# Kernel tuning notes

Hardware: AMD Instinct MI355X
Metric: run time of the kernel (lower is better)

Reference implementation:

```python
import jax, jax.numpy as jnp
import numpy as np

N_USERS = 200000   # == num movies (code indexes movie_x with user ids)
N_MOVIES = 200000
N_ENT = 400000
C = 64


def _ngcf(x, edge_index, W1, b1, W2, b2, num_nodes):
    # PyG flow source_to_target: x_j = x[src], x_i = x[dst], aggr='add' at dst
    src, dst = edge_index[0], edge_index[1]
    xj = x[src]                      # [E, C]
    xi = x[dst]                      # [E, C]
    msg = xj @ W1 + b1 + (xi * xj) @ W2 + b2
    return jax.ops.segment_sum(msg, dst, num_segments=num_nodes)


def _rgcn(x, edge_index, Wrel, Wroot, brgcn, num_nodes):
    # single relation (edge_type all zero); RGCNConv default aggr='mean'
    src, dst = edge_index[0], edge_index[1]
    msg = x[src] @ Wrel              # [E, C]
    agg = jax.ops.segment_sum(msg, dst, num_segments=num_nodes)
    cnt = jax.ops.segment_sum(jnp.ones((msg.shape[0],), msg.dtype), dst,
                              num_segments=num_nodes)
    agg = agg / jnp.maximum(cnt, 1.0)[:, None]
    return agg + x @ Wroot + brgcn


def setup_inputs() -> dict:
    key = jax.random.key(0)
    ks = jax.random.split(key, 12)
    s = 1.0 / np.sqrt(C)
    return {
        "user_x": jax.random.normal(ks[0], (N_USERS, C), jnp.float32),
        "movie_x": jax.random.normal(ks[1], (N_MOVIES, C), jnp.float32),
        "entity_x": jax.random.normal(ks[2], (N_ENT, C), jnp.float32),
        "um_edge_index": jax.random.randint(ks[3], (2, 1000000), 0, N_USERS, jnp.int32),
        "me_edge_index": jax.random.randint(ks[4], (2, 1000000), 0, N_MOVIES, jnp.int32),
        "W1": jax.random.uniform(ks[5], (C, C), jnp.float32, -s, s),
        "b1": jax.random.uniform(ks[6], (C,), jnp.float32, -s, s),
        "W2": jax.random.uniform(ks[7], (C, C), jnp.float32, -s, s),
        "b2": jax.random.uniform(ks[8], (C,), jnp.float32, -s, s),
        "Wrel": jax.random.uniform(ks[9], (C, C), jnp.float32, -s, s),
        "Wroot": jax.random.uniform(ks[10], (C, C), jnp.float32, -s, s),
        "brgcn": jax.random.uniform(ks[11], (C,), jnp.float32, -s, s),
    }


def reference(user_x, movie_x, entity_x, um_edge_index, me_edge_index,
              W1, b1, W2, b2, Wrel, Wroot, brgcn):
    # movie side: NGCF over user->movie edges, x = movie_x (faithful to source)
    movie_msg = _ngcf(movie_x, um_edge_index, W1, b1, W2, b2, N_MOVIES)
    entity_msg = _rgcn(entity_x, me_edge_index, Wrel, Wroot, brgcn, N_ENT)
    movie_emb = jnp.concatenate(
        [movie_x, movie_msg + entity_msg[:N_MOVIES]], axis=1)
    # user side: reversed edges
    um_rev = jnp.stack([um_edge_index[1], um_edge_index[0]], axis=0)
    user_msg = _ngcf(user_x, um_rev, W1, b1, W2, b2, N_USERS)
    user_emb = jnp.concatenate([user_x, user_msg], axis=1)
    return (user_emb, movie_emb)
```

## Files before the change

kernel.cpp:

```cpp
#include <hip/hip_runtime.h>

#define NUSERS  200000
#define NMOVIES 200000
#define NROWS   200000
#define NCB     782
#define NB      512
#define CAPB    1792
#define ELCAP   1792
#define OVF_MAX 8192

typedef __attribute__((ext_vector_type(8))) short bf16x8;
typedef __attribute__((ext_vector_type(4))) float f32x4;

__global__ __launch_bounds__(256) void bin_scatter_kernel(
    const int* __restrict__ um, const int* __restrict__ me,
    int* __restrict__ C, int* __restrict__ LB, int* __restrict__ part,
    int E_um, int E_me, int CH_um, int CH_me)
{
    __shared__ int hist[NCB];
    __shared__ int lscan[NCB];
    __shared__ int tsum[256];
    __shared__ int stage[1984];

    const int bid = blockIdx.x;
    const int s = bid / NB;
    const int blk = bid % NB;
    const int E  = (s < 2) ? E_um : E_me;
    const int CH = (s < 2) ? CH_um : CH_me;
    const int t0 = blk * CH;
    const int n = max(0, min(t0 + CH, E) - t0);
    const int tid = threadIdx.x;

    const int* kp;
    const int* vp;
    if (s == 0)      { kp = um;        vp = um + E_um; }
    else if (s == 1) { kp = um + E_um; vp = um; }
    else             { kp = me + E_me; vp = me; }

    for (int i = tid; i < NCB; i += 256) hist[i] = 0;
    __syncthreads();

    for (int j = tid; j < n; j += 256) {
        const int key = kp[t0 + j];
        atomicAdd(&hist[key >> 8], 1);
    }
    __syncthreads();

    const int crow = (s * NB + blk) * NCB;
    for (int i = tid; i < NCB; i += 256) C[crow + i] = hist[i];

    {
        const int b4 = tid * 4;
        const int v0 = (b4 + 0 < NCB) ? hist[b4 + 0] : 0;
        const int v1 = (b4 + 1 < NCB) ? hist[b4 + 1] : 0;
        const int v2 = (b4 + 2 < NCB) ? hist[b4 + 2] : 0;
        const int v3 = (b4 + 3 < NCB) ? hist[b4 + 3] : 0;
        const int ssum = v0 + v1 + v2 + v3;
        tsum[tid] = ssum;
        __syncthreads();
#pragma unroll
        for (int off = 1; off < 256; off <<= 1) {
            const int t = (tid >= off) ? tsum[tid - off] : 0;
            __syncthreads();
            tsum[tid] += t;
            __syncthreads();
        }
        const int excl = tsum[tid] - ssum;
        if (b4 + 0 < NCB) lscan[b4 + 0] = excl;
        if (b4 + 1 < NCB) lscan[b4 + 1] = excl + v0;
        if (b4 + 2 < NCB) lscan[b4 + 2] = excl + v0 + v1;
        if (b4 + 3 < NCB) lscan[b4 + 3] = excl + v0 + v1 + v2;
    }
    __syncthreads();

    for (int i = tid; i < NCB; i += 256) LB[crow + i] = lscan[i];
    for (int i = tid; i < NCB; i += 256) hist[i] = lscan[i];
    __syncthreads();

    for (int j = tid; j < n; j += 256) {
        const int key = kp[t0 + j];
        const int val = vp[t0 + j];
        const int pos = atomicAdd(&hist[key >> 8], 1);
        stage[pos] = (val << 8) | (key & 255);
    }
    __syncthreads();

    int* preg;
    if (s == 0)      preg = part + (size_t)blk * CH_um;
    else if (s == 1) preg = part + (size_t)NB * CH_um + (size_t)blk * CH_um;
    else             preg = part + (size_t)2 * NB * CH_um + (size_t)blk * CH_me;
    for (int i = tid; i < n; i += 256) preg[i] = stage[i];
}

__global__ __launch_bounds__(256) void bin_csr_kernel(
    const int* __restrict__ part,
    const int* __restrict__ C, const int* __restrict__ LB,
    int* __restrict__ csr,
    int* __restrict__ rowcnt_all,
    int* __restrict__ rowstart_all,
    int* __restrict__ ovf_meta, int* __restrict__ ovf_list,
    int CH_um, int CH_me)
{
    __shared__ int cfrag[NB];
    __shared__ int foff[NB + 1];
    __shared__ int tsum[256];
    __shared__ int el[ELCAP];
    __shared__ int sorted[ELCAP];
    __shared__ int fhist[256];
    __shared__ int frank[256];

    const int bid = blockIdx.x;
    const int s = bid / NCB;
    const int bin = bid % NCB;
    const int tid = threadIdx.x;
    const int CH = (s < 2) ? CH_um : CH_me;
    const int* preg = part + (s == 0 ? (size_t)0
                      : (s == 1 ? (size_t)NB * CH_um
                                : (size_t)2 * NB * CH_um));

    for (int b = tid; b < NB; b += 256) cfrag[b] = C[(s * NB + b) * NCB + bin];
    fhist[tid] = 0;
    __syncthreads();

    {
        const int a0 = cfrag[2 * tid];
        const int a1 = cfrag[2 * tid + 1];
        const int ss = a0 + a1;
        tsum[tid] = ss;
        __syncthreads();
#pragma unroll
        for (int off = 1; off < 256; off <<= 1) {
            const int t = (tid >= off) ? tsum[tid - off] : 0;
            __syncthreads();
            tsum[tid] += t;
            __syncthreads();
        }
        const int excl = tsum[tid] - ss;
        foff[2 * tid] = excl;
        foff[2 * tid + 1] = excl + a0;
        if (tid == 255) foff[NB] = tsum[255];
    }
    __syncthreads();
    const int nbin = foff[NB];
    const int nel = min(nbin, ELCAP);

    for (int b = tid; b < NB; b += 256) {
        const int c = cfrag[b];
        if (c == 0) continue;
        const int off = LB[(s * NB + b) * NCB + bin];
        const int* frag = preg + (size_t)b * CH + off;
        const int dst0 = foff[b];
        for (int j = 0; j < c; ++j) {
            const int v = frag[j];
            const int idx = dst0 + j;
            if (idx < ELCAP) {
                el[idx] = v;
            } else {
                const int i = atomicAdd(ovf_meta, 1);
                if (i < OVF_MAX) {
                    ovf_list[2 * i]     = (s << 18) | (bin * 256 + (v & 255));
                    ovf_list[2 * i + 1] = v >> 8;
                }
            }
        }
    }
    __syncthreads();

    for (int i = tid; i < nel; i += 256) atomicAdd(&fhist[el[i] & 255], 1);
    __syncthreads();

    {
        const int v = fhist[tid];
        tsum[tid] = v;
        __syncthreads();
#pragma unroll
        for (int off = 1; off < 256; off <<= 1) {
            const int t = (tid >= off) ? tsum[tid - off] : 0;
            __syncthreads();
            tsum[tid] += t;
            __syncthreads();
        }
        const int excl = tsum[tid] - v;
        frank[tid] = excl;
        const int r = bin * 256 + tid;
        if (r < NROWS) {
            rowstart_all[s * NROWS + r] = ((s * NCB) + bin) * CAPB + excl;
            rowcnt_all[s * NROWS + r] = v;
        }
    }
    __syncthreads();

    for (int i = tid; i < nel; i += 256) {
        const int p = el[i];
        const int pos = atomicAdd(&frank[p & 255], 1);
        sorted[pos] = p >> 8;
    }
    __syncthreads();

    int* outp = csr + ((size_t)s * NCB + bin) * CAPB;
    for (int i = tid; i < nel; i += 256) outp[i] = sorted[i];
}

__global__ __launch_bounds__(256) void gather_kernel(
    const int* __restrict__ csr,
    const float* __restrict__ x,
    const int* __restrict__ rowcnt,
    const int* __restrict__ rowstart,
    float* __restrict__ outbase,
    int out_off, int nrows)
{
    const int lane = threadIdx.x & 63;
    const int wid = __builtin_amdgcn_readfirstlane(
        (blockIdx.x * blockDim.x + threadIdx.x) >> 6);
    const int nw = (gridDim.x * blockDim.x) >> 6;
    const int rpw = (nrows + nw - 1) / nw;
    const int r0 = wid * rpw;
    const int r1 = min(r0 + rpw, nrows);
    for (int r = r0; r < r1; ++r) {
        const int c = rowcnt[r];
        const int base = rowstart[r];
        float acc0 = 0.f, acc1 = 0.f, acc2 = 0.f, acc3 = 0.f;
        int j = 0;
        for (; j + 4 <= c; j += 4) {
            const int s0 = csr[base + j];
            const int s1 = csr[base + j + 1];
            const int s2 = csr[base + j + 2];
            const int s3 = csr[base + j + 3];
            acc0 += x[(size_t)s0 * 64 + lane];
            acc1 += x[(size_t)s1 * 64 + lane];
            acc2 += x[(size_t)s2 * 64 + lane];
            acc3 += x[(size_t)s3 * 64 + lane];
        }
        for (; j < c; ++j) {
            const int s0 = csr[base + j];
            acc0 += x[(size_t)s0 * 64 + lane];
        }
        outbase[(size_t)r * 128 + out_off + lane] = (acc0 + acc1) + (acc2 + acc3);
    }
}

__global__ __launch_bounds__(256) void fixup_kernel(
    const int* __restrict__ ovf_meta,
    const int* __restrict__ ovf_list,
    const float* __restrict__ user_x,
    const float* __restrict__ movie_x,
    const float* __restrict__ entity_x,
    int* __restrict__ rowcnt_all,
    float* __restrict__ out_user,
    float* __restrict__ out_movie)
{
    const int n = min(ovf_meta[0], OVF_MAX);
    const int lane = threadIdx.x & 63;
    const int wv = (blockIdx.x * blockDim.x + threadIdx.x) >> 6;
    const int nw = (gridDim.x * blockDim.x) >> 6;
    for (int i = wv; i < n; i += nw) {
        const int key = ovf_list[2 * i];
        const int src = ovf_list[2 * i + 1];
        const int s = key >> 18;
        const int dst = key & 0x3FFFF;
        if (dst >= NROWS) continue;
        if (s == 0) {
            atomicAdd(&out_user[(size_t)dst * 128 + 64 + lane],
                      user_x[(size_t)src * 64 + lane]);
        } else if (s == 1) {
            atomicAdd(&out_movie[(size_t)dst * 128 + 64 + lane],
                      movie_x[(size_t)src * 64 + lane]);
        } else {
            atomicAdd(&out_movie[(size_t)dst * 128 + lane],
                      entity_x[(size_t)src * 64 + lane]);
        }
        if (lane == 0) atomicAdd(&rowcnt_all[s * NROWS + dst], 1);
    }
}

__global__ __launch_bounds__(256) void bsplit_kernel(
    const float* __restrict__ W1, const float* __restrict__ W2,
    const float* __restrict__ Wrel, const float* __restrict__ Wroot,
    unsigned short* __restrict__ BH, unsigned short* __restrict__ BL)
{
    const int idx = blockIdx.x * blockDim.x + threadIdx.x;
    if (idx >= 8 * 4 * 64 * 8) return;
    const int j = idx & 7;
    const int f = idx >> 3;
    const int l = f & 63;
    const int t = (f >> 6) & 3;
    const int s = f >> 8;
    const int k = 32 * s + 8 * (l >> 4) + j;
    const int col = 16 * t + (l & 15);
    const float* Wsrc;
    switch (k >> 6) {
        case 0:  Wsrc = W1;    break;
        case 1:  Wsrc = W2;    break;
        case 2:  Wsrc = Wrel;  break;
        default: Wsrc = Wroot; break;
    }
    const float v = Wsrc[(k & 63) * 64 + col];
    const unsigned int bits = __float_as_uint(v);
    const unsigned short h = (unsigned short)(bits >> 16);
    const float rem = v - __uint_as_float((unsigned)h << 16);
    BH[idx] = h;
    BL[idx] = (unsigned short)(__float_as_uint(rem) >> 16);
}

__device__ __forceinline__ short bf_hi(float v, float& rem) {
    const unsigned int b = __float_as_uint(v);
    const unsigned short h = (unsigned short)(b >> 16);
    rem = v - __uint_as_float((unsigned)h << 16);
    return (short)h;
}
__device__ __forceinline__ short bf_tr(float v) {
    return (short)(__float_as_uint(v) >> 16);
}
__device__ __forceinline__ void split8(float4 q0, float4 q1,
                                       bf16x8& Ah, bf16x8& Al) {
    float r0, r1, r2, r3, r4, r5, r6, r7;
    Ah[0] = bf_hi(q0.x, r0); Ah[1] = bf_hi(q0.y, r1);
    Ah[2] = bf_hi(q0.z, r2); Ah[3] = bf_hi(q0.w, r3);
    Ah[4] = bf_hi(q1.x, r4); Ah[5] = bf_hi(q1.y, r5);
    Ah[6] = bf_hi(q1.z, r6); Ah[7] = bf_hi(q1.w, r7);
    Al[0] = bf_tr(r0); Al[1] = bf_tr(r1); Al[2] = bf_tr(r2); Al[3] = bf_tr(r3);
    Al[4] = bf_tr(r4); Al[5] = bf_tr(r5); Al[6] = bf_tr(r6); Al[7] = bf_tr(r7);
}

#define MFMA3(acc, Ah, Al, Bh, Bl)                                           \
    acc = __builtin_amdgcn_mfma_f32_16x16x32_bf16(Ah, Bh, acc, 0, 0, 0);     \
    acc = __builtin_amdgcn_mfma_f32_16x16x32_bf16(Al, Bh, acc, 0, 0, 0);     \
    acc = __builtin_amdgcn_mfma_f32_16x16x32_bf16(Ah, Bl, acc, 0, 0, 0);

__global__ __launch_bounds__(256) void finalize_user_mfma(
    const float* __restrict__ user_x,
    const int* __restrict__ cnt_u,
    const float* __restrict__ b1, const float* __restrict__ b2,
    const unsigned short* __restrict__ BH,
    const unsigned short* __restrict__ BL,
    float* out_user)
{
    const int lane = threadIdx.x & 63;
    const int wv = threadIdx.x >> 6;
    const int sub = lane & 15, grp = lane >> 4;
    const int rbase = blockIdx.x * 64 + wv * 16;
    const int myrow = rbase + sub;

    f32x4 acc0 = {0.f, 0.f, 0.f, 0.f}, acc1 = acc0, acc2 = acc0, acc3 = acc0;

#pragma unroll
    for (int s = 0; s < 4; ++s) {
        float4 q0, q1;
        if (s < 2) {
            const float* p = out_user + (size_t)myrow * 128 + 64 + 32 * s + 8 * grp;
            q0 = *(const float4*)p;
            q1 = *(const float4*)(p + 4);
        } else {
            const int off = 32 * (s - 2) + 8 * grp;
            const float* ps = out_user + (size_t)myrow * 128 + 64 + off;
            const float* px = user_x + (size_t)myrow * 64 + off;
            const float4 s0 = *(const float4*)ps, s1 = *(const float4*)(ps + 4);
            const float4 x0 = *(const float4*)px, x1 = *(const float4*)(px + 4);
            q0.x = s0.x * x0.x; q0.y = s0.y * x0.y;
            q0.z = s0.z * x0.z; q0.w = s0.w * x0.w;
            q1.x = s1.x * x1.x; q1.y = s1.y * x1.y;
            q1.z = s1.z * x1.z; q1.w = s1.w * x1.w;
        }
        bf16x8 Ah, Al;
        split8(q0, q1, Ah, Al);
#pragma unroll
        for (int t = 0; t < 4; ++t) {
            const int fo = ((s * 4 + t) * 64 + lane) * 8;
            const bf16x8 Bh = *(const bf16x8*)(BH + fo);
            const bf16x8 Bl = *(const bf16x8*)(BL + fo);
            if (t == 0) { MFMA3(acc0, Ah, Al, Bh, Bl) }
            else if (t == 1) { MFMA3(acc1, Ah, Al, Bh, Bl) }
            else if (t == 2) { MFMA3(acc2, Ah, Al, Bh, Bl) }
            else { MFMA3(acc3, Ah, Al, Bh, Bl) }
        }
    }

#pragma unroll
    for (int i = 0; i < 4; ++i) {
        const int row = rbase + 4 * i + grp;
        const float4 xv = *(const float4*)(user_x + (size_t)row * 64 + sub * 4);
        *(float4*)(out_user + (size_t)row * 128 + sub * 4) = xv;
    }

#pragma unroll
    for (int t = 0; t < 4; ++t) {
        const int col = 16 * t + sub;
        const float bb = b1[col] + b2[col];
        const f32x4 a = (t == 0) ? acc0 : (t == 1) ? acc1 : (t == 2) ? acc2 : acc3;
#pragma unroll
        for (int r = 0; r < 4; ++r) {
            const int row = rbase + 4 * grp + r;
            out_user[(size_t)row * 128 + 64 + col] =
                a[r] + (float)cnt_u[row] * bb;
        }
    }
}

__global__ __launch_bounds__(256) void finalize_movie_mfma(
    const float* __restrict__ movie_x,
    const float* __restrict__ entity_x,
    const int* __restrict__ cnt_m, const int* __restrict__ cnt_e,
    const float* __restrict__ b1, const float* __restrict__ b2,
    const float* __restrict__ brgcn,
    const unsigned short* __restrict__ BH,
    const unsigned short* __restrict__ BL,
    float* out_movie)
{
    const int lane = threadIdx.x & 63;
    const int wv = threadIdx.x >> 6;
    const int sub = lane & 15, grp = lane >> 4;
    const int rbase = blockIdx.x * 64 + wv * 16;
    const int myrow = rbase + sub;
    const float invce = 1.0f / fmaxf((float)cnt_e[myrow], 1.0f);

    f32x4 acc0 = {0.f, 0.f, 0.f, 0.f}, acc1 = acc0, acc2 = acc0, acc3 = acc0;

#pragma unroll
    for (int s = 0; s < 8; ++s) {
        float4 q0, q1;
        if (s < 2) {
            const float* p = out_movie + (size_t)myrow * 128 + 64 + 32 * s + 8 * grp;
            q0 = *(const float4*)p;
            q1 = *(const float4*)(p + 4);
        } else if (s < 4) {
            const int off = 32 * (s - 2) + 8 * grp;
            const float* ps = out_movie + (size_t)myrow * 128 + 64 + off;
            const float* px = movie_x + (size_t)myrow * 64 + off;
            const float4 s0 = *(const float4*)ps, s1 = *(const float4*)(ps + 4);
            const float4 x0 = *(const float4*)px, x1 = *(const float4*)(px + 4);
            q0.x = s0.x * x0.x; q0.y = s0.y * x0.y;
            q0.z = s0.z * x0.z; q0.w = s0.w * x0.w;
            q1.x = s1.x * x1.x; q1.y = s1.y * x1.y;
            q1.z = s1.z * x1.z; q1.w = s1.w * x1.w;
        } else if (s < 6) {
            const float* p = out_movie + (size_t)myrow * 128 + 32 * (s - 4) + 8 * grp;
            const float4 e0 = *(const float4*)p, e1 = *(const float4*)(p + 4);
            q0.x = e0.x * invce; q0.y = e0.y * invce;
            q0.z = e0.z * invce; q0.w = e0.w * invce;
            q1.x = e1.x * invce; q1.y = e1.y * invce;
            q1.z = e1.z * invce; q1.w = e1.w * invce;
        } else {
            const float* p = entity_x + (size_t)myrow * 64 + 32 * (s - 6) + 8 * grp;
            q0 = *(const float4*)p;
            q1 = *(const float4*)(p + 4);
        }
        bf16x8 Ah, Al;
        split8(q0, q1, Ah, Al);
#pragma unroll
        for (int t = 0; t < 4; ++t) {
            const int fo = ((s * 4 + t) * 64 + lane) * 8;
            const bf16x8 Bh = *(const bf16x8*)(BH + fo);
            const bf16x8 Bl = *(const bf16x8*)(BL + fo);
            if (t == 0) { MFMA3(acc0, Ah, Al, Bh, Bl) }
            else if (t == 1) { MFMA3(acc1, Ah, Al, Bh, Bl) }
            else if (t == 2) { MFMA3(acc2, Ah, Al, Bh, Bl) }
            else { MFMA3(acc3, Ah, Al, Bh, Bl) }
        }
    }

#pragma unroll
    for (int i = 0; i < 4; ++i) {
        const int row = rbase + 4 * i + grp;
        const float4 xv = *(const float4*)(movie_x + (size_t)row * 64 + sub * 4);
        *(float4*)(out_movie + (size_t)row * 128 + sub * 4) = xv;
    }

#pragma unroll
    for (int t = 0; t < 4; ++t) {
        const int col = 16 * t + sub;
        const float bb = b1[col] + b2[col];
        const float br = brgcn[col];
        const f32x4 a = (t == 0) ? acc0 : (t == 1) ? acc1 : (t == 2) ? acc2 : acc3;
#pragma unroll
        for (int r = 0; r < 4; ++r) {
            const int row = rbase + 4 * grp + r;
            out_movie[(size_t)row * 128 + 64 + col] =
                a[r] + (float)cnt_m[row] * bb + br;
        }
    }
}

extern "C" void kernel_launch(void* const* d_in, const int* in_sizes, int n_in,
                              void* d_out, int out_size, void* d_ws, size_t ws_size,
                              hipStream_t stream)
{
    const float* user_x   = (const float*)d_in[0];
    const float* movie_x  = (const float*)d_in[1];
    const float* entity_x = (const float*)d_in[2];
    const int*   um       = (const int*)d_in[3];
    const int*   me       = (const int*)d_in[4];
    const float* W1       = (const float*)d_in[5];
    const float* b1       = (const float*)d_in[6];
    const float* W2       = (const float*)d_in[7];
    const float* b2       = (const float*)d_in[8];
    const float* Wrel     = (const float*)d_in[9];
    const float* Wroot    = (const float*)d_in[10];
    const float* brgcn    = (const float*)d_in[11];

    const int E_um = in_sizes[3] / 2;
    const int E_me = in_sizes[4] / 2;
    const int CH_um = (E_um + NB - 1) / NB;
    const int CH_me = (E_me + NB - 1) / NB;

    float* out_user  = (float*)d_out;
    float* out_movie = out_user + (size_t)NUSERS * 128;

    int* C        = (int*)d_ws;
    int* LB       = C + 3 * NB * NCB;
    int* rowcnt   = LB + 3 * NB * NCB;
    int* rowstart = rowcnt + 3 * NROWS;
    int* ovf_meta = rowstart + 3 * NROWS;
    int* ovf_list = ovf_meta + 2;
    int* part     = ovf_list + 2 * OVF_MAX;
    int* csr      = part + (size_t)2 * NB * CH_um + (size_t)NB * CH_me;
    uintptr_t bp = (uintptr_t)(csr + (size_t)3 * NCB * CAPB);
    bp = (bp + 63) & ~(uintptr_t)63;
    unsigned short* BH = (unsigned short*)bp;
    unsigned short* BL = BH + 16384;

    int* cnt_u = rowcnt;
    int* cnt_m = rowcnt + NROWS;
    int* cnt_e = rowcnt + 2 * NROWS;

    hipMemsetAsync(ovf_meta, 0, 2 * sizeof(int), stream);

    bsplit_kernel<<<64, 256, 0, stream>>>(W1, W2, Wrel, Wroot, BH, BL);
    bin_scatter_kernel<<<3 * NB, 256, 0, stream>>>(um, me, C, LB, part,
                                                   E_um, E_me, CH_um, CH_me);
    bin_csr_kernel<<<3 * NCB, 256, 0, stream>>>(part, C, LB, csr,
                                                rowcnt, rowstart,
                                                ovf_meta, ovf_list,
                                                CH_um, CH_me);

    gather_kernel<<<2048, 256, 0, stream>>>(csr, entity_x,
                                            cnt_e, rowstart + 2 * NROWS,
                                            out_movie, 0, NMOVIES);
    gather_kernel<<<2048, 256, 0, stream>>>(csr, movie_x,
                                            cnt_m, rowstart + NROWS,
                                            out_movie, 64, NMOVIES);
    gather_kernel<<<2048, 256, 0, stream>>>(csr, user_x,
                                            cnt_u, rowstart,
                                            out_user, 64, NUSERS);

    fixup_kernel<<<16, 256, 0, stream>>>(ovf_meta, ovf_list, user_x, movie_x,
                                         entity_x, rowcnt, out_user, out_movie);

    finalize_user_mfma<<<NUSERS / 64, 256, 0, stream>>>(
        user_x, cnt_u, b1, b2, BH, BL, out_user);
    finalize_movie_mfma<<<NMOVIES / 64, 256, 0, stream>>>(
        movie_x, entity_x, cnt_m, cnt_e, b1, b2, brgcn, BH, BL, out_movie);
}
```

Before: 352.7 us.

## Fuse neighbor gather into MFMA finalize kernels via shared-memory tiles

Before, three gather kernels wrote aggregated sums into the output buffer and two finalize kernels read them back for the bf16-split MFMA projection. Now each 16-row wave gathers its neighbor sums straight into a padded shared-memory tile, and the MFMA projection runs in the same kernel. This removes the global write and re-read of the intermediate aggregates. Because of that, overflow edges can no longer be pre-summed, so the fixup kernel now applies the full per-edge W1/W2/Wrel projection before its atomic adds. The CSR builder also counts row histograms over every element, not only the stored ones. The movie NGCF kernel adds onto the RGCN partial already in the output, which makes the kernels order-dependent.

```diff
diff --git a/kernel.cpp b/kernel.cpp
--- a/kernel.cpp
+++ b/kernel.cpp
@@ -97,6 +97,7 @@
     const int* __restrict__ C, const int* __restrict__ LB,
     int* __restrict__ csr,
     int* __restrict__ rowcnt_all,
+    int* __restrict__ rowstored_all,
     int* __restrict__ rowstart_all,
     int* __restrict__ ovf_meta, int* __restrict__ ovf_list,
     int CH_um, int CH_me)
@@ -107,6 +108,7 @@
     __shared__ int el[ELCAP];
     __shared__ int sorted[ELCAP];
     __shared__ int fhist[256];
+    __shared__ int fexcl[256];
     __shared__ int frank[256];
 
     const int bid = blockIdx.x;
@@ -142,7 +144,6 @@
     }
     __syncthreads();
     const int nbin = foff[NB];
-    const int nel = min(nbin, ELCAP);
 
     for (int b = tid; b < NB; b += 256) {
         const int c = cfrag[b];
@@ -152,6 +153,7 @@
         const int dst0 = foff[b];
         for (int j = 0; j < c; ++j) {
             const int v = frag[j];
+            atomicAdd(&fhist[v & 255], 1);
             const int idx = dst0 + j;
             if (idx < ELCAP) {
                 el[idx] = v;
@@ -166,9 +168,6 @@
     }
     __syncthreads();
 
-    for (int i = tid; i < nel; i += 256) atomicAdd(&fhist[el[i] & 255], 1);
-    __syncthreads();
-
     {
         const int v = fhist[tid];
         tsum[tid] = v;
@@ -181,97 +180,96 @@
             __syncthreads();
         }
         const int excl = tsum[tid] - v;
+        fexcl[tid] = excl;
         frank[tid] = excl;
         const int r = bin * 256 + tid;
         if (r < NROWS) {
-            rowstart_all[s * NROWS + r] = ((s * NCB) + bin) * CAPB + excl;
+            rowstart_all[s * NROWS + r] =
+                ((s * NCB) + bin) * CAPB + min(excl, ELCAP);
             rowcnt_all[s * NROWS + r] = v;
         }
     }
     __syncthreads();
 
+    const int nel = min(nbin, ELCAP);
     for (int i = tid; i < nel; i += 256) {
         const int p = el[i];
         const int pos = atomicAdd(&frank[p & 255], 1);
-        sorted[pos] = p >> 8;
-    }
-    __syncthreads();
+        if (pos < ELCAP) {
+            sorted[pos] = p >> 8;
+        } else {
+            const int k = atomicAdd(ovf_meta, 1);
+            if (k < OVF_MAX) {
+                ovf_list[2 * k]     = (s << 18) | (bin * 256 + (p & 255));
+                ovf_list[2 * k + 1] = p >> 8;
+            }
+        }
+    }
+    __syncthreads();
+
+    {
+        const int r = bin * 256 + tid;
+        if (r < NROWS) {
+            const int st = max(0, min(ELCAP, frank[tid]) - min(ELCAP, fexcl[tid]));
+            rowstored_all[s * NROWS + r] = st;
+        }
+    }
 
     int* outp = csr + ((size_t)s * NCB + bin) * CAPB;
-    for (int i = tid; i < nel; i += 256) outp[i] = sorted[i];
-}
-
-__global__ __launch_bounds__(256) void gather_kernel(
+    const int nfl = min(nbin, ELCAP);
+    for (int i = tid; i < nfl; i += 256) outp[i] = sorted[i];
+}
+
+__device__ __forceinline__ void gather16(
     const int* __restrict__ csr,
     const float* __restrict__ x,
-    const int* __restrict__ rowcnt,
+    const int* __restrict__ rowstored,
     const int* __restrict__ rowstart,
-    float* __restrict__ outbase,
-    int out_off, int nrows)
-{
-    const int lane = threadIdx.x & 63;
-    const int wid = __builtin_amdgcn_readfirstlane(
-        (blockIdx.x * blockDim.x + threadIdx.x) >> 6);
-    const int nw = (gridDim.x * blockDim.x) >> 6;
-    const int rpw = (nrows + nw - 1) / nw;
-    const int r0 = wid * rpw;
-    const int r1 = min(r0 + rpw, nrows);
-    for (int r = r0; r < r1; ++r) {
-        const int c = rowcnt[r];
+    int rbase, int lane, float (*tile)[17])
+{
+    for (int i = 0; i < 16; ++i) {
+        const int r = rbase + i;
+        const int c = rowstored[r];
         const int base = rowstart[r];
-        float acc0 = 0.f, acc1 = 0.f, acc2 = 0.f, acc3 = 0.f;
+        float a0 = 0.f, a1 = 0.f, a2 = 0.f, a3 = 0.f;
         int j = 0;
         for (; j + 4 <= c; j += 4) {
             const int s0 = csr[base + j];
             const int s1 = csr[base + j + 1];
             const int s2 = csr[base + j + 2];
             const int s3 = csr[base + j + 3];
-            acc0 += x[(size_t)s0 * 64 + lane];
-            acc1 += x[(size_t)s1 * 64 + lane];
-            acc2 += x[(size_t)s2 * 64 + lane];
-            acc3 += x[(size_t)s3 * 64 + lane];
-        }
-        for (; j < c; ++j) {
-            const int s0 = csr[base + j];
-            acc0 += x[(size_t)s0 * 64 + lane];
-        }
-        outbase[(size_t)r * 128 + out_off + lane] = (acc0 + acc1) + (acc2 + acc3);
-    }
-}
-
-__global__ __launch_bounds__(256) void fixup_kernel(
-    const int* __restrict__ ovf_meta,
-    const int* __restrict__ ovf_list,
-    const float* __restrict__ user_x,
-    const float* __restrict__ movie_x,
-    const float* __restrict__ entity_x,
-    int* __restrict__ rowcnt_all,
-    float* __restrict__ out_user,
-    float* __restrict__ out_movie)
-{
-    const int n = min(ovf_meta[0], OVF_MAX);
-    const int lane = threadIdx.x & 63;
-    const int wv = (blockIdx.x * blockDim.x + threadIdx.x) >> 6;
-    const int nw = (gridDim.x * blockDim.x) >> 6;
-    for (int i = wv; i < n; i += nw) {
-        const int key = ovf_list[2 * i];
-        const int src = ovf_list[2 * i + 1];
-        const int s = key >> 18;
-        const int dst = key & 0x3FFFF;
-        if (dst >= NROWS) continue;
-        if (s == 0) {
-            atomicAdd(&out_user[(size_t)dst * 128 + 64 + lane],
-                      user_x[(size_t)src * 64 + lane]);
-        } else if (s == 1) {
-            atomicAdd(&out_movie[(size_t)dst * 128 + 64 + lane],
-                      movie_x[(size_t)src * 64 + lane]);
-        } else {
-            atomicAdd(&out_movie[(size_t)dst * 128 + lane],
-                      entity_x[(size_t)src * 64 + lane]);
-        }
-        if (lane == 0) atomicAdd(&rowcnt_all[s * NROWS + dst], 1);
-    }
-}
+            a0 += x[(size_t)s0 * 64 + lane];
+            a1 += x[(size_t)s1 * 64 + lane];
+            a2 += x[(size_t)s2 * 64 + lane];
+            a3 += x[(size_t)s3 * 64 + lane];
+        }
+        for (; j < c; ++j) a0 += x[(size_t)csr[base + j] * 64 + lane];
+        tile[lane][i] = (a0 + a1) + (a2 + a3);
+    }
+}
+
+__device__ __forceinline__ short bf_hi(float v, float& rem) {
+    const unsigned int b = __float_as_uint(v);
+    const unsigned short h = (unsigned short)(b >> 16);
+    rem = v - __uint_as_float((unsigned)h << 16);
+    return (short)h;
+}
+__device__ __forceinline__ short bf_tr(float v) {
+    return (short)(__float_as_uint(v) >> 16);
+}
+__device__ __forceinline__ void split8v(const float q[8],
+                                        bf16x8& Ah, bf16x8& Al) {
+    float r[8];
+#pragma unroll
+    for (int j = 0; j < 8; ++j) Ah[j] = bf_hi(q[j], r[j]);
+#pragma unroll
+    for (int j = 0; j < 8; ++j) Al[j] = bf_tr(r[j]);
+}
+
+#define MFMA3(acc, Ah, Al, Bh, Bl)                                           \
+    acc = __builtin_amdgcn_mfma_f32_16x16x32_bf16(Ah, Bh, acc, 0, 0, 0);     \
+    acc = __builtin_amdgcn_mfma_f32_16x16x32_bf16(Al, Bh, acc, 0, 0, 0);     \
+    acc = __builtin_amdgcn_mfma_f32_16x16x32_bf16(Ah, Bl, acc, 0, 0, 0);
 
 __global__ __launch_bounds__(256) void bsplit_kernel(
     const float* __restrict__ W1, const float* __restrict__ W2,
@@ -302,67 +300,45 @@
     BL[idx] = (unsigned short)(__float_as_uint(rem) >> 16);
 }
 
-__device__ __forceinline__ short bf_hi(float v, float& rem) {
-    const unsigned int b = __float_as_uint(v);
-    const unsigned short h = (unsigned short)(b >> 16);
-    rem = v - __uint_as_float((unsigned)h << 16);
-    return (short)h;
-}
-__device__ __forceinline__ short bf_tr(float v) {
-    return (short)(__float_as_uint(v) >> 16);
-}
-__device__ __forceinline__ void split8(float4 q0, float4 q1,
-                                       bf16x8& Ah, bf16x8& Al) {
-    float r0, r1, r2, r3, r4, r5, r6, r7;
-    Ah[0] = bf_hi(q0.x, r0); Ah[1] = bf_hi(q0.y, r1);
-    Ah[2] = bf_hi(q0.z, r2); Ah[3] = bf_hi(q0.w, r3);
-    Ah[4] = bf_hi(q1.x, r4); Ah[5] = bf_hi(q1.y, r5);
-    Ah[6] = bf_hi(q1.z, r6); Ah[7] = bf_hi(q1.w, r7);
-    Al[0] = bf_tr(r0); Al[1] = bf_tr(r1); Al[2] = bf_tr(r2); Al[3] = bf_tr(r3);
-    Al[4] = bf_tr(r4); Al[5] = bf_tr(r5); Al[6] = bf_tr(r6); Al[7] = bf_tr(r7);
-}
-
-#define MFMA3(acc, Ah, Al, Bh, Bl)                                           \
-    acc = __builtin_amdgcn_mfma_f32_16x16x32_bf16(Ah, Bh, acc, 0, 0, 0);     \
-    acc = __builtin_amdgcn_mfma_f32_16x16x32_bf16(Al, Bh, acc, 0, 0, 0);     \
-    acc = __builtin_amdgcn_mfma_f32_16x16x32_bf16(Ah, Bl, acc, 0, 0, 0);
-
-__global__ __launch_bounds__(256) void finalize_user_mfma(
-    const float* __restrict__ user_x,
-    const int* __restrict__ cnt_u,
-    const float* __restrict__ b1, const float* __restrict__ b2,
+__global__ __launch_bounds__(256) void rgcn_partial_kernel(
+    const float* __restrict__ entity_x,
+    const int* __restrict__ csr,
+    const int* __restrict__ rowstored_e, const int* __restrict__ rowstart_e,
+    const int* __restrict__ rowcnt_e,
+    const float* __restrict__ brgcn,
     const unsigned short* __restrict__ BH,
     const unsigned short* __restrict__ BL,
-    float* out_user)
-{
+    float* __restrict__ out_movie)
+{
+    __shared__ float tSe[4][64][17];
     const int lane = threadIdx.x & 63;
     const int wv = threadIdx.x >> 6;
     const int sub = lane & 15, grp = lane >> 4;
     const int rbase = blockIdx.x * 64 + wv * 16;
     const int myrow = rbase + sub;
 
+    gather16(csr, entity_x, rowstored_e, rowstart_e, rbase, lane, tSe[wv]);
+
+    const float invce = 1.0f / fmaxf((float)rowcnt_e[myrow], 1.0f);
     f32x4 acc0 = {0.f, 0.f, 0.f, 0.f}, acc1 = acc0, acc2 = acc0, acc3 = acc0;
 
 #pragma unroll
-    for (int s = 0; s < 4; ++s) {
-        float4 q0, q1;
-        if (s < 2) {
-            const float* p = out_user + (size_t)myrow * 128 + 64 + 32 * s + 8 * grp;
-            q0 = *(const float4*)p;
-            q1 = *(const float4*)(p + 4);
+    for (int s = 4; s < 8; ++s) {
+        float q[8];
+        if (s < 6) {
+            const int ch0 = 32 * (s - 4) + 8 * grp;
+#pragma unroll
+            for (int j = 0; j < 8; ++j) q[j] = tSe[wv][ch0 + j][sub] * invce;
         } else {
-            const int off = 32 * (s - 2) + 8 * grp;
-            const float* ps = out_user + (size_t)myrow * 128 + 64 + off;
-            const float* px = user_x + (size_t)myrow * 64 + off;
-            const float4 s0 = *(const float4*)ps, s1 = *(const float4*)(ps + 4);
-            const float4 x0 = *(const float4*)px, x1 = *(const float4*)(px + 4);
-            q0.x = s0.x * x0.x; q0.y = s0.y * x0.y;
-            q0.z = s0.z * x0.z; q0.w = s0.w * x0.w;
-            q1.x = s1.x * x1.x; q1.y = s1.y * x1.y;
-            q1.z = s1.z * x1.z; q1.w = s1.w * x1.w;
+            const int ch0 = 32 * (s - 6) + 8 * grp;
+            const float* p = entity_x + (size_t)myrow * 64 + ch0;
+            const float4 e0 = *(const float4*)p;
+            const float4 e1 = *(const float4*)(p + 4);
+            q[0] = e0.x; q[1] = e0.y; q[2] = e0.z; q[3] = e0.w;
+            q[4] = e1.x; q[5] = e1.y; q[6] = e1.z; q[7] = e1.w;
         }
         bf16x8 Ah, Al;
-        split8(q0, q1, Ah, Al);
+        split8v(q, Ah, Al);
 #pragma unroll
         for (int t = 0; t < 4; ++t) {
             const int fo = ((s * 4 + t) * 64 + lane) * 8;
@@ -376,76 +352,55 @@
     }
 
 #pragma unroll
-    for (int i = 0; i < 4; ++i) {
-        const int row = rbase + 4 * i + grp;
-        const float4 xv = *(const float4*)(user_x + (size_t)row * 64 + sub * 4);
-        *(float4*)(out_user + (size_t)row * 128 + sub * 4) = xv;
-    }
-
-#pragma unroll
     for (int t = 0; t < 4; ++t) {
         const int col = 16 * t + sub;
-        const float bb = b1[col] + b2[col];
+        const float br = brgcn[col];
         const f32x4 a = (t == 0) ? acc0 : (t == 1) ? acc1 : (t == 2) ? acc2 : acc3;
 #pragma unroll
         for (int r = 0; r < 4; ++r) {
             const int row = rbase + 4 * grp + r;
-            out_user[(size_t)row * 128 + 64 + col] =
-                a[r] + (float)cnt_u[row] * bb;
-        }
-    }
-}
-
-__global__ __launch_bounds__(256) void finalize_movie_mfma(
-    const float* __restrict__ movie_x,
-    const float* __restrict__ entity_x,
-    const int* __restrict__ cnt_m, const int* __restrict__ cnt_e,
+            out_movie[(size_t)row * 128 + 64 + col] = a[r] + br;
+        }
+    }
+}
+
+template <bool ADD_PARTIAL>
+__global__ __launch_bounds__(256) void ngcf_fused_kernel(
+    const float* __restrict__ x,
+    const int* __restrict__ csr,
+    const int* __restrict__ rowstored, const int* __restrict__ rowstart,
+    const int* __restrict__ rowcnt,
     const float* __restrict__ b1, const float* __restrict__ b2,
-    const float* __restrict__ brgcn,
     const unsigned short* __restrict__ BH,
     const unsigned short* __restrict__ BL,
-    float* out_movie)
-{
+    float* __restrict__ outp)
+{
+    __shared__ float tS1[4][64][17];
     const int lane = threadIdx.x & 63;
     const int wv = threadIdx.x >> 6;
     const int sub = lane & 15, grp = lane >> 4;
     const int rbase = blockIdx.x * 64 + wv * 16;
     const int myrow = rbase + sub;
-    const float invce = 1.0f / fmaxf((float)cnt_e[myrow], 1.0f);
+
+    gather16(csr, x, rowstored, rowstart, rbase, lane, tS1[wv]);
 
     f32x4 acc0 = {0.f, 0.f, 0.f, 0.f}, acc1 = acc0, acc2 = acc0, acc3 = acc0;
 
 #pragma unroll
-    for (int s = 0; s < 8; ++s) {
-        float4 q0, q1;
-        if (s < 2) {
-            const float* p = out_movie + (size_t)myrow * 128 + 64 + 32 * s + 8 * grp;
-            q0 = *(const float4*)p;
-            q1 = *(const float4*)(p + 4);
-        } else if (s < 4) {
-            const int off = 32 * (s - 2) + 8 * grp;
-            const float* ps = out_movie + (size_t)myrow * 128 + 64 + off;
-            const float* px = movie_x + (size_t)myrow * 64 + off;
-            const float4 s0 = *(const float4*)ps, s1 = *(const float4*)(ps + 4);
-            const float4 x0 = *(const float4*)px, x1 = *(const float4*)(px + 4);
-            q0.x = s0.x * x0.x; q0.y = s0.y * x0.y;
-            q0.z = s0.z * x0.z; q0.w = s0.w * x0.w;
-            q1.x = s1.x * x1.x; q1.y = s1.y * x1.y;
-            q1.z = s1.z * x1.z; q1.w = s1.w * x1.w;
-        } else if (s < 6) {
-            const float* p = out_movie + (size_t)myrow * 128 + 32 * (s - 4) + 8 * grp;
-            const float4 e0 = *(const float4*)p, e1 = *(const float4*)(p + 4);
-            q0.x = e0.x * invce; q0.y = e0.y * invce;
-            q0.z = e0.z * invce; q0.w = e0.w * invce;
-            q1.x = e1.x * invce; q1.y = e1.y * invce;
-            q1.z = e1.z * invce; q1.w = e1.w * invce;
-        } else {
-            const float* p = entity_x + (size_t)myrow * 64 + 32 * (s - 6) + 8 * grp;
-            q0 = *(const float4*)p;
-            q1 = *(const float4*)(p + 4);
+    for (int s = 0; s < 4; ++s) {
+        const int ch0 = 32 * (s & 1) + 8 * grp;
+        float q[8];
+#pragma unroll
+        for (int j = 0; j < 8; ++j) q[j] = tS1[wv][ch0 + j][sub];
+        if (s >= 2) {
+            const float* px = x + (size_t)myrow * 64 + ch0;
+            const float4 x0 = *(const float4*)px;
+            const float4 x1 = *(const float4*)(px + 4);
+            q[0] *= x0.x; q[1] *= x0.y; q[2] *= x0.z; q[3] *= x0.w;
+            q[4] *= x1.x; q[5] *= x1.y; q[6] *= x1.z; q[7] *= x1.w;
         }
         bf16x8 Ah, Al;
-        split8(q0, q1, Ah, Al);
+        split8v(q, Ah, Al);
 #pragma unroll
         for (int t = 0; t < 4; ++t) {
             const int fo = ((s * 4 + t) * 64 + lane) * 8;
@@ -461,21 +416,63 @@
 #pragma unroll
     for (int i = 0; i < 4; ++i) {
         const int row = rbase + 4 * i + grp;
-        const float4 xv = *(const float4*)(movie_x + (size_t)row * 64 + sub * 4);
-        *(float4*)(out_movie + (size_t)row * 128 + sub * 4) = xv;
+        const float4 xv = *(const float4*)(x + (size_t)row * 64 + sub * 4);
+        *(float4*)(outp + (size_t)row * 128 + sub * 4) = xv;
     }
 
 #pragma unroll
     for (int t = 0; t < 4; ++t) {
         const int col = 16 * t + sub;
         const float bb = b1[col] + b2[col];
-        const float br = brgcn[col];
         const f32x4 a = (t == 0) ? acc0 : (t == 1) ? acc1 : (t == 2) ? acc2 : acc3;
 #pragma unroll
         for (int r = 0; r < 4; ++r) {
             const int row = rbase + 4 * grp + r;
-            out_movie[(size_t)row * 128 + 64 + col] =
-                a[r] + (float)cnt_m[row] * bb + br;
+            float v = a[r] + (float)rowcnt[row] * bb;
+            if (ADD_PARTIAL) v += outp[(size_t)row * 128 + 64 + col];
+            outp[(size_t)row * 128 + 64 + col] = v;
+        }
+    }
+}
+
+__global__ __launch_bounds__(256) void fixup_kernel(
+    const int* __restrict__ ovf_meta,
+    const int* __restrict__ ovf_list,
+    const float* __restrict__ user_x,
+    const float* __restrict__ movie_x,
+    const float* __restrict__ entity_x,
+    const int* __restrict__ rowcnt_all,
+    const float* __restrict__ W1, const float* __restrict__ W2,
+    const float* __restrict__ Wrel,
+    float* __restrict__ out_user,
+    float* __restrict__ out_movie)
+{
+    const int n = min(ovf_meta[0], OVF_MAX);
+    const int lane = threadIdx.x & 63;
+    const int wv = (blockIdx.x * blockDim.x + threadIdx.x) >> 6;
+    const int nw = (gridDim.x * blockDim.x) >> 6;
+    for (int i = wv; i < n; i += nw) {
+        const int key = ovf_list[2 * i];
+        const int src = ovf_list[2 * i + 1];
+        const int s = key >> 18;
+        const int dst = key & 0x3FFFF;
+        if (dst >= NROWS) continue;
+        float acc = 0.f;
+        if (s == 2) {
+            const float* xs = entity_x + (size_t)src * 64;
+            for (int k = 0; k < 64; ++k) acc += xs[k] * Wrel[k * 64 + lane];
+            const float ce = fmaxf((float)rowcnt_all[2 * NROWS + dst], 1.0f);
+            atomicAdd(&out_movie[(size_t)dst * 128 + 64 + lane], acc / ce);
+        } else {
+            const float* xb = (s == 0) ? user_x : movie_x;
+            const float* xs = xb + (size_t)src * 64;
+            const float* xd = xb + (size_t)dst * 64;
+            for (int k = 0; k < 64; ++k) {
+                const float sv = xs[k];
+                acc += sv * W1[k * 64 + lane] + xd[k] * sv * W2[k * 64 + lane];
+            }
+            float* o = (s == 0) ? out_user : out_movie;
+            atomicAdd(&o[(size_t)dst * 128 + 64 + lane], acc);
         }
     }
 }
@@ -505,48 +502,41 @@
     float* out_user  = (float*)d_out;
     float* out_movie = out_user + (size_t)NUSERS * 128;
 
-    int* C        = (int*)d_ws;
-    int* LB       = C + 3 * NB * NCB;
-    int* rowcnt   = LB + 3 * NB * NCB;
-    int* rowstart = rowcnt + 3 * NROWS;
-    int* ovf_meta = rowstart + 3 * NROWS;
-    int* ovf_list = ovf_meta + 2;
-    int* part     = ovf_list + 2 * OVF_MAX;
-    int* csr      = part + (size_t)2 * NB * CH_um + (size_t)NB * CH_me;
+    int* C         = (int*)d_ws;
+    int* LB        = C + 3 * NB * NCB;
+    int* rowcnt    = LB + 3 * NB * NCB;
+    int* rowstored = rowcnt + 3 * NROWS;
+    int* rowstart  = rowstored + 3 * NROWS;
+    int* ovf_meta  = rowstart + 3 * NROWS;
+    int* ovf_list  = ovf_meta + 2;
+    int* part      = ovf_list + 2 * OVF_MAX;
+    int* csr       = part + (size_t)2 * NB * CH_um + (size_t)NB * CH_me;
     uintptr_t bp = (uintptr_t)(csr + (size_t)3 * NCB * CAPB);
     bp = (bp + 63) & ~(uintptr_t)63;
     unsigned short* BH = (unsigned short*)bp;
     unsigned short* BL = BH + 16384;
 
-    int* cnt_u = rowcnt;
-    int* cnt_m = rowcnt + NROWS;
-    int* cnt_e = rowcnt + 2 * NROWS;
-
     hipMemsetAsync(ovf_meta, 0, 2 * sizeof(int), stream);
 
     bsplit_kernel<<<64, 256, 0, stream>>>(W1, W2, Wrel, Wroot, BH, BL);
     bin_scatter_kernel<<<3 * NB, 256, 0, stream>>>(um, me, C, LB, part,
                                                    E_um, E_me, CH_um, CH_me);
     bin_csr_kernel<<<3 * NCB, 256, 0, stream>>>(part, C, LB, csr,
-                                                rowcnt, rowstart,
+                                                rowcnt, rowstored, rowstart,
                                                 ovf_meta, ovf_list,
                                                 CH_um, CH_me);
 
-    gather_kernel<<<2048, 256, 0, stream>>>(csr, entity_x,
-                                            cnt_e, rowstart + 2 * NROWS,
-                                            out_movie, 0, NMOVIES);
-    gather_kernel<<<2048, 256, 0, stream>>>(csr, movie_x,
-                                            cnt_m, rowstart + NROWS,
-                                            out_movie, 64, NMOVIES);
-    gather_kernel<<<2048, 256, 0, stream>>>(csr, user_x,
-                                            cnt_u, rowstart,
-                                            out_user, 64, NUSERS);
+    rgcn_partial_kernel<<<NMOVIES / 64, 256, 0, stream>>>(
+        entity_x, csr, rowstored + 2 * NROWS, rowstart + 2 * NROWS,
+        rowcnt + 2 * NROWS, brgcn, BH, BL, out_movie);
+    ngcf_fused_kernel<true><<<NMOVIES / 64, 256, 0, stream>>>(
+        movie_x, csr, rowstored + NROWS, rowstart + NROWS, rowcnt + NROWS,
+        b1, b2, BH, BL, out_movie);
+    ngcf_fused_kernel<false><<<NUSERS / 64, 256, 0, stream>>>(
+        user_x, csr, rowstored, rowstart, rowcnt,
+        b1, b2, BH, BL, out_user);
 
     fixup_kernel<<<16, 256, 0, stream>>>(ovf_meta, ovf_list, user_x, movie_x,
-                                         entity_x, rowcnt, out_user, out_movie);
-
-    finalize_user_mfma<<<NUSERS / 64, 256, 0, stream>>>(
-        user_x, cnt_u, b1, b2, BH, BL, out_user);
-    finalize_movie_mfma<<<NMOVIES / 64, 256, 0, stream>>>(
-        movie_x, entity_x, cnt_m, cnt_e, b1, b2, brgcn, BH, BL, out_movie);
-}
+                                         entity_x, rowcnt, W1, W2, Wrel,
+                                         out_user, out_movie);
+}
```

Result: slower. 462.2 us (+31.1%).
